# Kernel optimization log

Measured on AMD Instinct MI355X. Metric: run time of the kernel, lower is better.

Reference implementation:

```python
import jax, jax.numpy as jnp
import numpy as np

SLOT_DIM, EMB_DIM, HID, ACT_DIM, NUM_ACT = 256, 256, 1024, 128, 1024
EPS_SAMPLE = 1e-6
EPS_LN = 1e-5


def setup_inputs() -> dict:
    key = jax.random.key(0)
    ks = jax.random.split(key, 12)
    B, N, S = 128, 32, 12
    s = 0.02
    return {
        "slots": jax.random.normal(ks[0], (B, N, S, SLOT_DIM), jnp.float32),
        "noise": jax.random.normal(ks[1], (B, N - 1, S, ACT_DIM), jnp.float32),
        "W1": jax.random.normal(ks[2], (SLOT_DIM, HID), jnp.float32) * s,
        "b1": jnp.zeros((HID,), jnp.float32),
        "ln_g": jnp.ones((HID,), jnp.float32),
        "ln_b": jnp.zeros((HID,), jnp.float32),
        "W2": jax.random.normal(ks[3], (HID, EMB_DIM), jnp.float32) * s,
        "b2": jnp.zeros((EMB_DIM,), jnp.float32),
        "Wm": jax.random.normal(ks[4], (EMB_DIM, ACT_DIM), jnp.float32) * s,
        "bm": jnp.zeros((ACT_DIM,), jnp.float32),
        "Wv": jax.random.normal(ks[5], (EMB_DIM, ACT_DIM), jnp.float32) * s,
        "bv": jnp.zeros((ACT_DIM,), jnp.float32),
        "codebook": jax.random.normal(ks[6], (NUM_ACT, ACT_DIM), jnp.float32) * s,
    }


def reference(slots, noise, W1, b1, ln_g, ln_b, W2, b2, Wm, bm, Wv, bv, codebook):
    sg = jax.lax.stop_gradient
    B, N, S, _ = slots.shape
    # per-slot MLP encoder: Linear -> ReLU -> LayerNorm -> Linear
    h = jax.nn.relu(jnp.einsum('bnsd,dh->bnsh', slots, W1) + b1)
    mu = h.mean(-1, keepdims=True)
    var = h.var(-1, keepdims=True)
    h = (h - mu) * jax.lax.rsqrt(var + EPS_LN) * ln_g + ln_b
    e = jnp.einsum('bnsh,he->bnse', h, W2) + b2  # (B,N,S,emb)
    # action distribution from consecutive frames
    mean_tok = jnp.einsum('bnse,ea->bnsa', e, Wm) + bm
    var_tok = jnp.abs(jnp.einsum('bnse,ea->bnsa', e, Wv) + bv)
    adm = mean_tok[:, 1:] - mean_tok[:, :-1]  # (B,N-1,S,A)
    adv = var_tok[:, 1:] + var_tok[:, :-1]
    action_dist = jnp.stack([adm, adv], axis=2)  # (B,N-1,2,S,A)
    # reparameterized sample
    z = noise * jnp.sqrt(adv + EPS_SAMPLE) + adm
    # VQ: nearest codebook entry via squared L2 distances
    zf = z.reshape(-1, ACT_DIM)  # (M,A)
    d = (jnp.sum(zf * zf, axis=1, keepdims=True)
         - 2.0 * zf @ codebook.T
         + jnp.sum(codebook * codebook, axis=1))  # (M,num_actions)
    idx = jnp.argmin(d, axis=1)  # (M,)
    q = codebook[idx].reshape(z.shape)
    quant_loss = jnp.mean((sg(z) - q) ** 2)
    commit_loss = jnp.mean((z - sg(q)) ** 2)
    q_st = z + sg(q - z)  # straight-through action prototypes
    action_variability = z - sg(q)
    action_idxs = idx.reshape(B, N - 1, S, 1)
    return (action_dist, z, action_variability, q_st, action_idxs, quant_loss, commit_loss)
```

## Files before the change

kernel.cpp:

```cpp
#include <hip/hip_runtime.h>
#include <math.h>

#define R_ROWS 49152
#define HID 1024
#define SLOT 256
#define EMB 256
#define ACT 128
#define NCODE 1024
#define M_ROWS 47616

#define OFF_AD 0
#define OFF_Z  12189696
#define OFF_AV 18284544
#define OFF_QS 24379392
#define OFF_IDX 30474240
#define OFF_QL 30521856
#define OFF_CL 30521857

#define WS_XH    0
#define WS_XL    6291456
#define WS_MT   12582912
#define WS_VT   18874368
#define WS_W1H  25165824
#define WS_W1L  25296896
#define WS_W2H  25427968
#define WS_W2L  25559040
#define WS_WMH  25690112
#define WS_WML  25706496
#define WS_WVH  25722880
#define WS_WVL  25739264
#define WS_CBH  25755648
#define WS_CBL  25821184
#define WS_CN   25886720
#define WS_LOSS 25887744

typedef _Float16 f16x8 __attribute__((ext_vector_type(8)));
typedef float f32x4 __attribute__((ext_vector_type(4)));

__device__ __forceinline__ void pack_body(
    const float* __restrict__ W, _Float16* __restrict__ hi, _Float16* __restrict__ lo,
    int lgS, int N, int p)
{
    int j = p & 7;
    int l = (p >> 3) & 63;
    int q = p >> 9;
    int s = q & ((1 << lgS) - 1);
    int t = q >> lgS;
    int n = t * 16 + (l & 15);
    int k = s * 32 + ((l >> 4) << 3) + j;
    float x = W[(size_t)k * N + n];
    _Float16 h = (_Float16)x;
    hi[p] = h;
    lo[p] = (_Float16)(x - (float)h);
}

__global__ __launch_bounds__(256) void k_packall(
    const float* __restrict__ W1, const float* __restrict__ W2,
    const float* __restrict__ Wm, const float* __restrict__ Wv,
    const float* __restrict__ CB, const float* __restrict__ X,
    _Float16* __restrict__ W1h, _Float16* __restrict__ W1l,
    _Float16* __restrict__ W2h, _Float16* __restrict__ W2l,
    _Float16* __restrict__ Wmh, _Float16* __restrict__ Wml,
    _Float16* __restrict__ Wvh, _Float16* __restrict__ Wvl,
    _Float16* __restrict__ CBh, _Float16* __restrict__ CBl,
    _Float16* __restrict__ Xh, _Float16* __restrict__ Xl,
    float* __restrict__ cn, float* __restrict__ losss)
{
    const int bi = blockIdx.x;
    const int tid = threadIdx.x;
    if (bi == 0 && tid == 0) *losss = 0.f;

    if (bi < 1024) {
        pack_body(W1, W1h, W1l, 3, HID, bi * 256 + tid);
    } else if (bi < 2048) {
        pack_body(W2, W2h, W2l, 5, EMB, (bi - 1024) * 256 + tid);
    } else if (bi < 2176) {
        pack_body(Wm, Wmh, Wml, 3, ACT, (bi - 2048) * 256 + tid);
    } else if (bi < 2304) {
        pack_body(Wv, Wvh, Wvl, 3, ACT, (bi - 2176) * 256 + tid);
    } else if (bi < 2816) {
        int p = (bi - 2304) * 256 + tid;
        int j = p & 7;
        int l = (p >> 3) & 63;
        int q = p >> 9;
        int s = q & 7;
        int t = q >> 3;
        int n = t * 32 + (l & 31);
        int k = s * 16 + ((l >> 5) << 3) + j;
        float x = CB[(size_t)n * ACT + k];
        _Float16 h = (_Float16)x;
        CBh[p] = h;
        CBl[p] = (_Float16)(x - (float)h);
    } else if (bi < 2820) {
        int c = (bi - 2816) * 256 + tid;
        float s = 0.f;
        #pragma unroll
        for (int k = 0; k < ACT; k += 4) {
            float4 v = *(const float4*)&CB[(size_t)c * ACT + k];
            s += v.x*v.x + v.y*v.y + v.z*v.z + v.w*v.w;
        }
        cn[c] = s;
    } else {
        size_t e0 = ((size_t)(bi - 2820) * 256 + tid) * 8;
        float4 va = *(const float4*)&X[e0];
        float4 vb = *(const float4*)&X[e0 + 4];
        float xv[8] = {va.x, va.y, va.z, va.w, vb.x, vb.y, vb.z, vb.w};
        f16x8 h8, l8;
        #pragma unroll
        for (int e = 0; e < 8; ++e) {
            _Float16 h = (_Float16)xv[e];
            h8[e] = h;
            l8[e] = (_Float16)(xv[e] - (float)h);
        }
        *(f16x8*)&Xh[e0] = h8;
        *(f16x8*)&Xl[e0] = l8;
    }
}

__global__ __launch_bounds__(512, 4) void k_encoder_mfma(
    const _Float16* __restrict__ Xh, const _Float16* __restrict__ Xl,
    const float* __restrict__ b1, const float* __restrict__ ln_g, const float* __restrict__ ln_b,
    const float* __restrict__ b2, const float* __restrict__ bm, const float* __restrict__ bv,
    const _Float16* __restrict__ W1h, const _Float16* __restrict__ W1l,
    const _Float16* __restrict__ W2h, const _Float16* __restrict__ W2l,
    const _Float16* __restrict__ Wmh, const _Float16* __restrict__ Wml,
    const _Float16* __restrict__ Wvh, const _Float16* __restrict__ Wvl,
    float* __restrict__ MT, float* __restrict__ VT)
{
    __shared__ _Float16 Hh0[16][1024];
    __shared__ _Float16 Hh1[16][1024];

    const int tid = threadIdx.x;
    const int w  = tid >> 6;
    const int l  = tid & 63;
    const int lr = l & 15;
    const int lg = l >> 4;
    const long rowbase = (long)blockIdx.x * 16;

    f16x8 a0[8], a1[8];
    {
        const _Float16* xh = Xh + (size_t)(rowbase + lr) * SLOT + lg * 8;
        const _Float16* xl = Xl + (size_t)(rowbase + lr) * SLOT + lg * 8;
        #pragma unroll
        for (int s = 0; s < 8; ++s) {
            a0[s] = *(const f16x8*)&xh[32 * s];
            a1[s] = *(const f16x8*)&xl[32 * s];
        }
    }

    f32x4 acc[8];
    #pragma unroll
    for (int t = 0; t < 8; ++t) acc[t] = (f32x4){0.f, 0.f, 0.f, 0.f};

    #pragma unroll
    for (int s = 0; s < 8; ++s) {
        #pragma unroll
        for (int t = 0; t < 8; ++t) {
            int tg = w * 8 + t;
            f16x8 bh = *(const f16x8*)(W1h + ((size_t)(tg * 8 + s) * 64 + l) * 8);
            f16x8 bl = *(const f16x8*)(W1l + ((size_t)(tg * 8 + s) * 64 + l) * 8);
            acc[t] = __builtin_amdgcn_mfma_f32_16x16x32_f16(a0[s], bh, acc[t], 0, 0, 0);
            acc[t] = __builtin_amdgcn_mfma_f32_16x16x32_f16(a0[s], bl, acc[t], 0, 0, 0);
            acc[t] = __builtin_amdgcn_mfma_f32_16x16x32_f16(a1[s], bh, acc[t], 0, 0, 0);
        }
    }

    #pragma unroll
    for (int t = 0; t < 8; ++t) {
        float bb = b1[w * 128 + t * 16 + lr];
        #pragma unroll
        for (int r = 0; r < 4; ++r) acc[t][r] = fmaxf(acc[t][r] + bb, 0.f);
    }

    float sum[4] = {0,0,0,0}, sq[4] = {0,0,0,0};
    #pragma unroll
    for (int t = 0; t < 8; ++t)
        #pragma unroll
        for (int r = 0; r < 4; ++r) {
            float v = acc[t][r];
            sum[r] += v; sq[r] = fmaf(v, v, sq[r]);
        }
    #pragma unroll
    for (int off = 1; off < 16; off <<= 1)
        #pragma unroll
        for (int r = 0; r < 4; ++r) {
            sum[r] += __shfl_xor(sum[r], off, 64);
            sq[r]  += __shfl_xor(sq[r],  off, 64);
        }
    float* stat = (float*)&Hh0[0][0];
    if (lr == 0) {
        #pragma unroll
        for (int r = 0; r < 4; ++r) {
            stat[w * 16 + 4 * lg + r]       = sum[r];
            stat[128 + w * 16 + 4 * lg + r] = sq[r];
        }
    }
    __syncthreads();
    float mu[4], rs[4];
    #pragma unroll
    for (int r = 0; r < 4; ++r) {
        int m = 4 * lg + r;
        float s = 0.f, q = 0.f;
        #pragma unroll
        for (int wv = 0; wv < 8; ++wv) {
            s += stat[wv * 16 + m];
            q += stat[128 + wv * 16 + m];
        }
        float mmu = s * (1.f / HID);
        float var = q * (1.f / HID) - mmu * mmu;
        mu[r] = mmu;
        rs[r] = 1.f / sqrtf(var + 1e-5f);
    }
    __syncthreads();

    #pragma unroll
    for (int t = 0; t < 8; ++t) {
        int n = w * 128 + t * 16 + lr;
        float g = ln_g[n], be = ln_b[n];
        #pragma unroll
        for (int r = 0; r < 4; ++r) {
            int m = 4 * lg + r;
            float v = (acc[t][r] - mu[r]) * rs[r] * g + be;
            _Float16 h = (_Float16)v;
            _Float16 lo = (_Float16)(v - (float)h);
            int c = n >> 3, jj = n & 7;
            int cs = c ^ (m & 7);
            Hh0[m][cs * 8 + jj] = h;
            Hh1[m][cs * 8 + jj] = lo;
        }
    }
    __syncthreads();

    f32x4 acc2[2];
    #pragma unroll
    for (int t = 0; t < 2; ++t) acc2[t] = (f32x4){0.f, 0.f, 0.f, 0.f};

    #pragma unroll 4
    for (int s = 0; s < 32; ++s) {
        int cs = (4 * s + lg) ^ (lr & 7);
        f16x8 ah = *(const f16x8*)&Hh0[lr][cs * 8];
        f16x8 al = *(const f16x8*)&Hh1[lr][cs * 8];
        #pragma unroll
        for (int t = 0; t < 2; ++t) {
            int tg = w * 2 + t;
            f16x8 bh = *(const f16x8*)(W2h + ((size_t)(tg * 32 + s) * 64 + l) * 8);
            f16x8 bl = *(const f16x8*)(W2l + ((size_t)(tg * 32 + s) * 64 + l) * 8);
            acc2[t] = __builtin_amdgcn_mfma_f32_16x16x32_f16(ah, bh, acc2[t], 0, 0, 0);
            acc2[t] = __builtin_amdgcn_mfma_f32_16x16x32_f16(ah, bl, acc2[t], 0, 0, 0);
            acc2[t] = __builtin_amdgcn_mfma_f32_16x16x32_f16(al, bh, acc2[t], 0, 0, 0);
        }
    }
    __syncthreads();

    _Float16* Es0 = &Hh0[0][0];
    _Float16* Es1 = &Hh0[0][0] + 4096;
    #pragma unroll
    for (int t = 0; t < 2; ++t) {
        int n = w * 32 + t * 16 + lr;
        float bb2 = b2[n];
        #pragma unroll
        for (int r = 0; r < 4; ++r) {
            int m = 4 * lg + r;
            float v = acc2[t][r] + bb2;
            _Float16 h = (_Float16)v;
            _Float16 lo = (_Float16)(v - (float)h);
            int c = n >> 3, jj = n & 7;
            int cs = c ^ (m & 7);
            Es0[m * 256 + cs * 8 + jj] = h;
            Es1[m * 256 + cs * 8 + jj] = lo;
        }
    }
    __syncthreads();

    const _Float16* WXh = (w < 4) ? Wmh : Wvh;
    const _Float16* WXl = (w < 4) ? Wml : Wvl;
    f32x4 acc3[2];
    #pragma unroll
    for (int t = 0; t < 2; ++t) acc3[t] = (f32x4){0.f, 0.f, 0.f, 0.f};

    #pragma unroll
    for (int s = 0; s < 8; ++s) {
        int cs = (4 * s + lg) ^ (lr & 7);
        f16x8 ah = *(const f16x8*)&Es0[lr * 256 + cs * 8];
        f16x8 al = *(const f16x8*)&Es1[lr * 256 + cs * 8];
        #pragma unroll
        for (int t = 0; t < 2; ++t) {
            int tg = (w & 3) * 2 + t;
            f16x8 bh = *(const f16x8*)(WXh + ((size_t)(tg * 8 + s) * 64 + l) * 8);
            f16x8 bl = *(const f16x8*)(WXl + ((size_t)(tg * 8 + s) * 64 + l) * 8);
            acc3[t] = __builtin_amdgcn_mfma_f32_16x16x32_f16(ah, bh, acc3[t], 0, 0, 0);
            acc3[t] = __builtin_amdgcn_mfma_f32_16x16x32_f16(ah, bl, acc3[t], 0, 0, 0);
            acc3[t] = __builtin_amdgcn_mfma_f32_16x16x32_f16(al, bh, acc3[t], 0, 0, 0);
        }
    }

    #pragma unroll
    for (int t = 0; t < 2; ++t) {
        int a = (w & 3) * 32 + t * 16 + lr;
        float bx = (w < 4) ? bm[a] : bv[a];
        #pragma unroll
        for (int r = 0; r < 4; ++r) {
            float v = acc3[t][r] + bx;
            size_t row = rowbase + 4 * lg + r;
            if (w < 4) MT[row * ACT + a] = v;
            else       VT[row * ACT + a] = fabsf(v);
        }
    }
}

__global__ __launch_bounds__(256, 2) void k_vqfused(
    const float* __restrict__ MT, const float* __restrict__ VT,
    const float* __restrict__ noise,
    const _Float16* __restrict__ CBh, const _Float16* __restrict__ CBl,
    const float* __restrict__ cn, const float* __restrict__ CB,
    float* __restrict__ out, float* __restrict__ losss)
{
    typedef float f32x16 __attribute__((ext_vector_type(16)));
    __shared__ float4 Zs4[4096];
    __shared__ int   idx_s[128];
    __shared__ float red[4];
    float* Zs = (float*)Zs4;

    const int tid = threadIdx.x;
    const int rowbase = blockIdx.x * 128;
    const int a = tid & 127;
    const int rhalf = tid >> 7;

    #pragma unroll 8
    for (int i = 0; i < 64; ++i) {
        int row = 2 * i + rhalf;
        int m = rowbase + row;
        int b = m / 372;
        int r1 = m + 12 * b;
        int r2 = r1 + 12;
        float m1 = MT[(size_t)r1 * ACT + a], m2 = MT[(size_t)r2 * ACT + a];
        float v1 = VT[(size_t)r1 * ACT + a], v2 = VT[(size_t)r2 * ACT + a];
        float adm = m2 - m1;
        float adv = v2 + v1;
        float z = noise[(size_t)m * ACT + a] * sqrtf(adv + 1e-6f) + adm;
        int np = m / 12, s = m - np * 12;
        out[OFF_AD + (size_t)(np * 24 + s) * ACT + a] = adm;
        out[OFF_AD + (size_t)(np * 24 + 12 + s) * ACT + a] = adv;
        out[OFF_Z + (size_t)m * ACT + a] = z;
        Zs[row * 128 + (((a >> 2) ^ (row & 31)) << 2) + (a & 3)] = z;
    }
    __syncthreads();

    const int w = tid >> 6, l = tid & 63;
    const int col = l & 31, hw = l >> 5;
    const int arow = 32 * w + col;

    f16x8 a0[8], a1[8];
    #pragma unroll
    for (int s = 0; s < 8; ++s) {
        #pragma unroll
        for (int half = 0; half < 2; ++half) {
            int k4 = s * 4 + hw * 2 + half;
            float4 v = *(const float4*)&Zs[arow * 128 + ((k4 ^ (arow & 31)) << 2)];
            float xv[4] = {v.x, v.y, v.z, v.w};
            #pragma unroll
            for (int e = 0; e < 4; ++e) {
                _Float16 h = (_Float16)xv[e];
                a0[s][half * 4 + e] = h;
                a1[s][half * 4 + e] = (_Float16)(xv[e] - (float)h);
            }
        }
    }

    float best[16];
    int bidx[16];
    #pragma unroll
    for (int r = 0; r < 16; ++r) { best[r] = 3.4e38f; bidx[r] = 0; }

    for (int cb = 0; cb < 4; ++cb) {
        f32x16 acc[8];
        #pragma unroll
        for (int t = 0; t < 8; ++t)
            #pragma unroll
            for (int r = 0; r < 16; ++r) acc[t][r] = 0.f;

        #pragma unroll
        for (int s = 0; s < 8; ++s) {
            #pragma unroll
            for (int t = 0; t < 8; ++t) {
                int tg = cb * 8 + t;
                f16x8 bh = *(const f16x8*)(CBh + ((size_t)(tg * 8 + s) * 64 + l) * 8);
                f16x8 bl = *(const f16x8*)(CBl + ((size_t)(tg * 8 + s) * 64 + l) * 8);
                acc[t] = __builtin_amdgcn_mfma_f32_32x32x16_f16(a0[s], bh, acc[t], 0, 0, 0);
                acc[t] = __builtin_amdgcn_mfma_f32_32x32x16_f16(a0[s], bl, acc[t], 0, 0, 0);
                acc[t] = __builtin_amdgcn_mfma_f32_32x32x16_f16(a1[s], bh, acc[t], 0, 0, 0);
            }
        }

        float cnv[8];
        #pragma unroll
        for (int t = 0; t < 8; ++t) cnv[t] = cn[cb * 256 + t * 32 + col];

        #pragma unroll
        for (int reg = 0; reg < 16; ++reg) {
            #pragma unroll
            for (int t = 0; t < 8; ++t) {
                float d = cnv[t] - 2.f * acc[t][reg];
                int gi = cb * 256 + t * 32 + col;
                if (d < best[reg]) { best[reg] = d; bidx[reg] = gi; }
            }
        }
    }

    #pragma unroll
    for (int reg = 0; reg < 16; ++reg) {
        float bv_ = best[reg];
        int bi_ = bidx[reg];
        #pragma unroll
        for (int off = 1; off < 32; off <<= 1) {
            float ov = __shfl_xor(bv_, off, 64);
            int   oi = __shfl_xor(bi_, off, 64);
            if (ov < bv_ || (ov == bv_ && oi < bi_)) { bv_ = ov; bi_ = oi; }
        }
        if (col == 0) {
            int mloc = 32 * w + (reg & 3) + 8 * (reg >> 2) + 4 * hw;
            idx_s[mloc] = bi_;
            out[OFF_IDX + rowbase + mloc] = (float)bi_;
        }
    }
    __syncthreads();

    float ls = 0.f;
    #pragma unroll 8
    for (int i = 0; i < 64; ++i) {
        int row = 2 * i + rhalf;
        float z = Zs[row * 128 + (((a >> 2) ^ (row & 31)) << 2) + (a & 3)];
        int ci = idx_s[row];
        float q = CB[(size_t)ci * ACT + a];
        float diff = z - q;
        size_t m = (size_t)(rowbase + row);
        out[OFF_QS + m * ACT + a] = z + (q - z);
        out[OFF_AV + m * ACT + a] = diff;
        ls = fmaf(diff, diff, ls);
    }
    #pragma unroll
    for (int off = 32; off; off >>= 1) ls += __shfl_xor(ls, off, 64);
    if (l == 0) red[w] = ls;
    __syncthreads();
    if (tid == 0) atomicAdd(losss, red[0] + red[1] + red[2] + red[3]);
}

__global__ void k_losses(const float* __restrict__ losss, float* __restrict__ out)
{
    float v = *losss * (1.f / 6094848.f);
    out[OFF_QL] = v;
    out[OFF_CL] = v;
}

extern "C" void kernel_launch(void* const* d_in, const int* in_sizes, int n_in,
                              void* d_out, int out_size, void* d_ws, size_t ws_size,
                              hipStream_t stream)
{
    const float* slots = (const float*)d_in[0];
    const float* noise = (const float*)d_in[1];
    const float* W1    = (const float*)d_in[2];
    const float* b1    = (const float*)d_in[3];
    const float* ln_g  = (const float*)d_in[4];
    const float* ln_b  = (const float*)d_in[5];
    const float* W2    = (const float*)d_in[6];
    const float* b2    = (const float*)d_in[7];
    const float* Wm    = (const float*)d_in[8];
    const float* bm    = (const float*)d_in[9];
    const float* Wv    = (const float*)d_in[10];
    const float* bv    = (const float*)d_in[11];
    const float* CB    = (const float*)d_in[12];
    float* out = (float*)d_out;
    float* ws  = (float*)d_ws;

    float* MT    = ws + WS_MT;
    float* VT    = ws + WS_VT;
    float* cn    = ws + WS_CN;
    float* losss = ws + WS_LOSS;

    _Float16* Xh  = (_Float16*)(ws + WS_XH);
    _Float16* Xl  = (_Float16*)(ws + WS_XL);
    _Float16* W1h = (_Float16*)(ws + WS_W1H);
    _Float16* W1l = (_Float16*)(ws + WS_W1L);
    _Float16* W2h = (_Float16*)(ws + WS_W2H);
    _Float16* W2l = (_Float16*)(ws + WS_W2L);
    _Float16* Wmh = (_Float16*)(ws + WS_WMH);
    _Float16* Wml = (_Float16*)(ws + WS_WML);
    _Float16* Wvh = (_Float16*)(ws + WS_WVH);
    _Float16* Wvl = (_Float16*)(ws + WS_WVL);
    _Float16* CBh = (_Float16*)(ws + WS_CBH);
    _Float16* CBl = (_Float16*)(ws + WS_CBL);

    hipLaunchKernelGGL(k_packall, dim3(8964), dim3(256), 0, stream,
                       W1, W2, Wm, Wv, CB, slots,
                       W1h, W1l, W2h, W2l, Wmh, Wml, Wvh, Wvl, CBh, CBl,
                       Xh, Xl, cn, losss);
    hipLaunchKernelGGL(k_encoder_mfma, dim3(R_ROWS/16), dim3(512), 0, stream,
                       Xh, Xl, b1, ln_g, ln_b, b2, bm, bv,
                       W1h, W1l, W2h, W2l, Wmh, Wml, Wvh, Wvl, MT, VT);
    hipLaunchKernelGGL(k_vqfused, dim3(M_ROWS/128), dim3(256), 0, stream,
                       MT, VT, noise, CBh, CBl, cn, CB, out, losss);
    hipLaunchKernelGGL(k_losses, dim3(1), dim3(1), 0, stream, losss, out);
}
```

Before: 443.9 us.

## Process 32 rows per encoder block with 16 waves to reuse weight fragments

The encoder kernel now handles 32 rows per block with 1024 threads instead of 16 rows with 512 threads. Each wave loads a weight fragment once and applies it to two 16-row tiles, halving the weight traffic per row across all three GEMM stages. LayerNorm statistics move to a dedicated shared buffer and are reduced by 32 threads. Shared memory doubles to about 136KB per block and there are half as many blocks, which may reduce occupancy and latency hiding. The launch bound of 1024 threads with min 4 blocks is also unlikely to be achievable.

```diff
diff --git a/kernel.cpp b/kernel.cpp
--- a/kernel.cpp
+++ b/kernel.cpp
@@ -117,7 +117,7 @@
     }
 }
 
-__global__ __launch_bounds__(512, 4) void k_encoder_mfma(
+__global__ __launch_bounds__(1024, 4) void k_encoder_mfma(
     const _Float16* __restrict__ Xh, const _Float16* __restrict__ Xl,
     const float* __restrict__ b1, const float* __restrict__ ln_g, const float* __restrict__ ln_b,
     const float* __restrict__ b2, const float* __restrict__ bm, const float* __restrict__ bv,
@@ -127,183 +127,215 @@
     const _Float16* __restrict__ Wvh, const _Float16* __restrict__ Wvl,
     float* __restrict__ MT, float* __restrict__ VT)
 {
-    __shared__ _Float16 Hh0[16][1024];
-    __shared__ _Float16 Hh1[16][1024];
+    __shared__ _Float16 Hh0[32][1024];
+    __shared__ _Float16 Hh1[32][1024];
+    __shared__ float stat_s[1024];
+    __shared__ float mu_s[32], rs_s[32];
 
     const int tid = threadIdx.x;
     const int w  = tid >> 6;
     const int l  = tid & 63;
     const int lr = l & 15;
     const int lg = l >> 4;
-    const long rowbase = (long)blockIdx.x * 16;
-
-    f16x8 a0[8], a1[8];
-    {
-        const _Float16* xh = Xh + (size_t)(rowbase + lr) * SLOT + lg * 8;
-        const _Float16* xl = Xl + (size_t)(rowbase + lr) * SLOT + lg * 8;
-        #pragma unroll
-        for (int s = 0; s < 8; ++s) {
-            a0[s] = *(const f16x8*)&xh[32 * s];
-            a1[s] = *(const f16x8*)&xl[32 * s];
-        }
-    }
-
-    f32x4 acc[8];
-    #pragma unroll
-    for (int t = 0; t < 8; ++t) acc[t] = (f32x4){0.f, 0.f, 0.f, 0.f};
+    const long rowbase = (long)blockIdx.x * 32;
+
+    f32x4 acc1[2][4];
+    #pragma unroll
+    for (int rt = 0; rt < 2; ++rt)
+        #pragma unroll
+        for (int t = 0; t < 4; ++t) acc1[rt][t] = (f32x4){0.f, 0.f, 0.f, 0.f};
 
     #pragma unroll
     for (int s = 0; s < 8; ++s) {
-        #pragma unroll
-        for (int t = 0; t < 8; ++t) {
-            int tg = w * 8 + t;
+        f16x8 a0[2], a1[2];
+        #pragma unroll
+        for (int rt = 0; rt < 2; ++rt) {
+            size_t xoff = (size_t)(rowbase + rt * 16 + lr) * SLOT + s * 32 + lg * 8;
+            a0[rt] = *(const f16x8*)&Xh[xoff];
+            a1[rt] = *(const f16x8*)&Xl[xoff];
+        }
+        #pragma unroll
+        for (int t = 0; t < 4; ++t) {
+            int tg = w * 4 + t;
             f16x8 bh = *(const f16x8*)(W1h + ((size_t)(tg * 8 + s) * 64 + l) * 8);
             f16x8 bl = *(const f16x8*)(W1l + ((size_t)(tg * 8 + s) * 64 + l) * 8);
-            acc[t] = __builtin_amdgcn_mfma_f32_16x16x32_f16(a0[s], bh, acc[t], 0, 0, 0);
-            acc[t] = __builtin_amdgcn_mfma_f32_16x16x32_f16(a0[s], bl, acc[t], 0, 0, 0);
-            acc[t] = __builtin_amdgcn_mfma_f32_16x16x32_f16(a1[s], bh, acc[t], 0, 0, 0);
-        }
-    }
-
-    #pragma unroll
-    for (int t = 0; t < 8; ++t) {
-        float bb = b1[w * 128 + t * 16 + lr];
-        #pragma unroll
-        for (int r = 0; r < 4; ++r) acc[t][r] = fmaxf(acc[t][r] + bb, 0.f);
-    }
-
-    float sum[4] = {0,0,0,0}, sq[4] = {0,0,0,0};
-    #pragma unroll
-    for (int t = 0; t < 8; ++t)
+            #pragma unroll
+            for (int rt = 0; rt < 2; ++rt) {
+                acc1[rt][t] = __builtin_amdgcn_mfma_f32_16x16x32_f16(a0[rt], bh, acc1[rt][t], 0, 0, 0);
+                acc1[rt][t] = __builtin_amdgcn_mfma_f32_16x16x32_f16(a0[rt], bl, acc1[rt][t], 0, 0, 0);
+                acc1[rt][t] = __builtin_amdgcn_mfma_f32_16x16x32_f16(a1[rt], bh, acc1[rt][t], 0, 0, 0);
+            }
+        }
+    }
+
+    #pragma unroll
+    for (int rt = 0; rt < 2; ++rt)
+        #pragma unroll
+        for (int t = 0; t < 4; ++t) {
+            float bb = b1[(w * 4 + t) * 16 + lr];
+            #pragma unroll
+            for (int r = 0; r < 4; ++r) acc1[rt][t][r] = fmaxf(acc1[rt][t][r] + bb, 0.f);
+        }
+
+    #pragma unroll
+    for (int rt = 0; rt < 2; ++rt) {
+        float sum[4] = {0,0,0,0}, sq[4] = {0,0,0,0};
+        #pragma unroll
+        for (int t = 0; t < 4; ++t)
+            #pragma unroll
+            for (int r = 0; r < 4; ++r) {
+                float v = acc1[rt][t][r];
+                sum[r] += v; sq[r] = fmaf(v, v, sq[r]);
+            }
+        #pragma unroll
+        for (int off = 1; off < 16; off <<= 1)
+            #pragma unroll
+            for (int r = 0; r < 4; ++r) {
+                sum[r] += __shfl_xor(sum[r], off, 64);
+                sq[r]  += __shfl_xor(sq[r],  off, 64);
+            }
+        if (lr == 0) {
+            #pragma unroll
+            for (int r = 0; r < 4; ++r) {
+                int row = rt * 16 + 4 * lg + r;
+                stat_s[w * 32 + row]       = sum[r];
+                stat_s[512 + w * 32 + row] = sq[r];
+            }
+        }
+    }
+    __syncthreads();
+
+    if (tid < 32) {
+        float s = 0.f, q = 0.f;
+        #pragma unroll
+        for (int wv = 0; wv < 16; ++wv) {
+            s += stat_s[wv * 32 + tid];
+            q += stat_s[512 + wv * 32 + tid];
+        }
+        float mu = s * (1.f / HID);
+        float var = q * (1.f / HID) - mu * mu;
+        mu_s[tid] = mu;
+        rs_s[tid] = 1.f / sqrtf(var + 1e-5f);
+    }
+    __syncthreads();
+
+    float murow[2][4], rsrow[2][4];
+    #pragma unroll
+    for (int rt = 0; rt < 2; ++rt)
         #pragma unroll
         for (int r = 0; r < 4; ++r) {
-            float v = acc[t][r];
-            sum[r] += v; sq[r] = fmaf(v, v, sq[r]);
-        }
-    #pragma unroll
-    for (int off = 1; off < 16; off <<= 1)
-        #pragma unroll
-        for (int r = 0; r < 4; ++r) {
-            sum[r] += __shfl_xor(sum[r], off, 64);
-            sq[r]  += __shfl_xor(sq[r],  off, 64);
-        }
-    float* stat = (float*)&Hh0[0][0];
-    if (lr == 0) {
-        #pragma unroll
-        for (int r = 0; r < 4; ++r) {
-            stat[w * 16 + 4 * lg + r]       = sum[r];
-            stat[128 + w * 16 + 4 * lg + r] = sq[r];
-        }
-    }
-    __syncthreads();
-    float mu[4], rs[4];
-    #pragma unroll
-    for (int r = 0; r < 4; ++r) {
-        int m = 4 * lg + r;
-        float s = 0.f, q = 0.f;
-        #pragma unroll
-        for (int wv = 0; wv < 8; ++wv) {
-            s += stat[wv * 16 + m];
-            q += stat[128 + wv * 16 + m];
-        }
-        float mmu = s * (1.f / HID);
-        float var = q * (1.f / HID) - mmu * mmu;
-        mu[r] = mmu;
-        rs[r] = 1.f / sqrtf(var + 1e-5f);
-    }
-    __syncthreads();
-
-    #pragma unroll
-    for (int t = 0; t < 8; ++t) {
-        int n = w * 128 + t * 16 + lr;
-        float g = ln_g[n], be = ln_b[n];
-        #pragma unroll
-        for (int r = 0; r < 4; ++r) {
-            int m = 4 * lg + r;
-            float v = (acc[t][r] - mu[r]) * rs[r] * g + be;
-            _Float16 h = (_Float16)v;
-            _Float16 lo = (_Float16)(v - (float)h);
+            int row = rt * 16 + 4 * lg + r;
+            murow[rt][r] = mu_s[row];
+            rsrow[rt][r] = rs_s[row];
+        }
+
+    #pragma unroll
+    for (int rt = 0; rt < 2; ++rt)
+        #pragma unroll
+        for (int t = 0; t < 4; ++t) {
+            int n = (w * 4 + t) * 16 + lr;
+            float g = ln_g[n], be = ln_b[n];
             int c = n >> 3, jj = n & 7;
-            int cs = c ^ (m & 7);
-            Hh0[m][cs * 8 + jj] = h;
-            Hh1[m][cs * 8 + jj] = lo;
-        }
-    }
+            #pragma unroll
+            for (int r = 0; r < 4; ++r) {
+                int row = rt * 16 + 4 * lg + r;
+                float v = (acc1[rt][t][r] - murow[rt][r]) * rsrow[rt][r] * g + be;
+                _Float16 h = (_Float16)v;
+                _Float16 lo = (_Float16)(v - (float)h);
+                int cs = c ^ (row & 7);
+                Hh0[row][cs * 8 + jj] = h;
+                Hh1[row][cs * 8 + jj] = lo;
+            }
+        }
     __syncthreads();
 
     f32x4 acc2[2];
     #pragma unroll
-    for (int t = 0; t < 2; ++t) acc2[t] = (f32x4){0.f, 0.f, 0.f, 0.f};
+    for (int rt = 0; rt < 2; ++rt) acc2[rt] = (f32x4){0.f, 0.f, 0.f, 0.f};
 
     #pragma unroll 4
     for (int s = 0; s < 32; ++s) {
-        int cs = (4 * s + lg) ^ (lr & 7);
-        f16x8 ah = *(const f16x8*)&Hh0[lr][cs * 8];
-        f16x8 al = *(const f16x8*)&Hh1[lr][cs * 8];
-        #pragma unroll
-        for (int t = 0; t < 2; ++t) {
-            int tg = w * 2 + t;
-            f16x8 bh = *(const f16x8*)(W2h + ((size_t)(tg * 32 + s) * 64 + l) * 8);
-            f16x8 bl = *(const f16x8*)(W2l + ((size_t)(tg * 32 + s) * 64 + l) * 8);
-            acc2[t] = __builtin_amdgcn_mfma_f32_16x16x32_f16(ah, bh, acc2[t], 0, 0, 0);
-            acc2[t] = __builtin_amdgcn_mfma_f32_16x16x32_f16(ah, bl, acc2[t], 0, 0, 0);
-            acc2[t] = __builtin_amdgcn_mfma_f32_16x16x32_f16(al, bh, acc2[t], 0, 0, 0);
+        f16x8 ah[2], al[2];
+        #pragma unroll
+        for (int rt = 0; rt < 2; ++rt) {
+            int row = rt * 16 + lr;
+            int cs = (s * 4 + lg) ^ (row & 7);
+            ah[rt] = *(const f16x8*)&Hh0[row][cs * 8];
+            al[rt] = *(const f16x8*)&Hh1[row][cs * 8];
+        }
+        f16x8 bh = *(const f16x8*)(W2h + ((size_t)(w * 32 + s) * 64 + l) * 8);
+        f16x8 bl = *(const f16x8*)(W2l + ((size_t)(w * 32 + s) * 64 + l) * 8);
+        #pragma unroll
+        for (int rt = 0; rt < 2; ++rt) {
+            acc2[rt] = __builtin_amdgcn_mfma_f32_16x16x32_f16(ah[rt], bh, acc2[rt], 0, 0, 0);
+            acc2[rt] = __builtin_amdgcn_mfma_f32_16x16x32_f16(ah[rt], bl, acc2[rt], 0, 0, 0);
+            acc2[rt] = __builtin_amdgcn_mfma_f32_16x16x32_f16(al[rt], bh, acc2[rt], 0, 0, 0);
         }
     }
     __syncthreads();
 
     _Float16* Es0 = &Hh0[0][0];
-    _Float16* Es1 = &Hh0[0][0] + 4096;
-    #pragma unroll
-    for (int t = 0; t < 2; ++t) {
-        int n = w * 32 + t * 16 + lr;
+    _Float16* Es1 = &Hh0[0][0] + 8192;
+    {
+        int n = w * 16 + lr;
         float bb2 = b2[n];
-        #pragma unroll
-        for (int r = 0; r < 4; ++r) {
-            int m = 4 * lg + r;
-            float v = acc2[t][r] + bb2;
-            _Float16 h = (_Float16)v;
-            _Float16 lo = (_Float16)(v - (float)h);
-            int c = n >> 3, jj = n & 7;
-            int cs = c ^ (m & 7);
-            Es0[m * 256 + cs * 8 + jj] = h;
-            Es1[m * 256 + cs * 8 + jj] = lo;
-        }
-    }
-    __syncthreads();
-
-    const _Float16* WXh = (w < 4) ? Wmh : Wvh;
-    const _Float16* WXl = (w < 4) ? Wml : Wvl;
+        int c = n >> 3, jj = n & 7;
+        #pragma unroll
+        for (int rt = 0; rt < 2; ++rt) {
+            #pragma unroll
+            for (int r = 0; r < 4; ++r) {
+                int row = rt * 16 + 4 * lg + r;
+                float v = acc2[rt][r] + bb2;
+                _Float16 h = (_Float16)v;
+                _Float16 lo = (_Float16)(v - (float)h);
+                int cs = c ^ (row & 7);
+                Es0[row * 256 + cs * 8 + jj] = h;
+                Es1[row * 256 + cs * 8 + jj] = lo;
+            }
+        }
+    }
+    __syncthreads();
+
+    const int half = w >> 3;
+    const int ct = w & 7;
+    const _Float16* WXh = half ? Wvh : Wmh;
+    const _Float16* WXl = half ? Wvl : Wml;
     f32x4 acc3[2];
     #pragma unroll
-    for (int t = 0; t < 2; ++t) acc3[t] = (f32x4){0.f, 0.f, 0.f, 0.f};
+    for (int rt = 0; rt < 2; ++rt) acc3[rt] = (f32x4){0.f, 0.f, 0.f, 0.f};
 
     #pragma unroll
     for (int s = 0; s < 8; ++s) {
-        int cs = (4 * s + lg) ^ (lr & 7);
-        f16x8 ah = *(const f16x8*)&Es0[lr * 256 + cs * 8];
-        f16x8 al = *(const f16x8*)&Es1[lr * 256 + cs * 8];
-        #pragma unroll
-        for (int t = 0; t < 2; ++t) {
-            int tg = (w & 3) * 2 + t;
-            f16x8 bh = *(const f16x8*)(WXh + ((size_t)(tg * 8 + s) * 64 + l) * 8);
-            f16x8 bl = *(const f16x8*)(WXl + ((size_t)(tg * 8 + s) * 64 + l) * 8);
-            acc3[t] = __builtin_amdgcn_mfma_f32_16x16x32_f16(ah, bh, acc3[t], 0, 0, 0);
-            acc3[t] = __builtin_amdgcn_mfma_f32_16x16x32_f16(ah, bl, acc3[t], 0, 0, 0);
-            acc3[t] = __builtin_amdgcn_mfma_f32_16x16x32_f16(al, bh, acc3[t], 0, 0, 0);
-        }
-    }
-
-    #pragma unroll
-    for (int t = 0; t < 2; ++t) {
-        int a = (w & 3) * 32 + t * 16 + lr;
-        float bx = (w < 4) ? bm[a] : bv[a];
-        #pragma unroll
-        for (int r = 0; r < 4; ++r) {
-            float v = acc3[t][r] + bx;
-            size_t row = rowbase + 4 * lg + r;
-            if (w < 4) MT[row * ACT + a] = v;
-            else       VT[row * ACT + a] = fabsf(v);
+        f16x8 ah[2], al[2];
+        #pragma unroll
+        for (int rt = 0; rt < 2; ++rt) {
+            int row = rt * 16 + lr;
+            int cs = (s * 4 + lg) ^ (row & 7);
+            ah[rt] = *(const f16x8*)&Es0[row * 256 + cs * 8];
+            al[rt] = *(const f16x8*)&Es1[row * 256 + cs * 8];
+        }
+        f16x8 bh = *(const f16x8*)(WXh + ((size_t)(ct * 8 + s) * 64 + l) * 8);
+        f16x8 bl = *(const f16x8*)(WXl + ((size_t)(ct * 8 + s) * 64 + l) * 8);
+        #pragma unroll
+        for (int rt = 0; rt < 2; ++rt) {
+            acc3[rt] = __builtin_amdgcn_mfma_f32_16x16x32_f16(ah[rt], bh, acc3[rt], 0, 0, 0);
+            acc3[rt] = __builtin_amdgcn_mfma_f32_16x16x32_f16(ah[rt], bl, acc3[rt], 0, 0, 0);
+            acc3[rt] = __builtin_amdgcn_mfma_f32_16x16x32_f16(al[rt], bh, acc3[rt], 0, 0, 0);
+        }
+    }
+
+    {
+        int a = ct * 16 + lr;
+        float bx = half ? bv[a] : bm[a];
+        #pragma unroll
+        for (int rt = 0; rt < 2; ++rt) {
+            #pragma unroll
+            for (int r = 0; r < 4; ++r) {
+                float v = acc3[rt][r] + bx;
+                size_t row = rowbase + rt * 16 + 4 * lg + r;
+                if (half) VT[row * ACT + a] = fabsf(v);
+                else      MT[row * ACT + a] = v;
+            }
         }
     }
 }
@@ -494,7 +526,7 @@
                        W1, W2, Wm, Wv, CB, slots,
                        W1h, W1l, W2h, W2l, Wmh, Wml, Wvh, Wvl, CBh, CBl,
                        Xh, Xl, cn, losss);
-    hipLaunchKernelGGL(k_encoder_mfma, dim3(R_ROWS/16), dim3(512), 0, stream,
+    hipLaunchKernelGGL(k_encoder_mfma, dim3(R_ROWS/32), dim3(1024), 0, stream,
                        Xh, Xl, b1, ln_g, ln_b, b2, bm, bv,
                        W1h, W1l, W2h, W2l, Wmh, Wml, Wvh, Wvl, MT, VT);
     hipLaunchKernelGGL(k_vqfused, dim3(M_ROWS/128), dim3(256), 0, stream,
```

Result: faster. 403.9 us (median of 2 runs) (-9.0%).
